# Performance work log

Measured on AMD Instinct MI355X. Metric: run time of the kernel, lower is better.

Reference implementation:

```python
import jax, jax.numpy as jnp
import numpy as np

IN_FEATURES = 8192
OUT_FEATURES = 8192
POOL_K = 16
SCALE = 2.0


def setup_inputs() -> dict:
    key = jax.random.key(0)
    k1, k2, k3 = jax.random.split(key, 3)
    B = 4096
    x = jax.random.normal(k1, (B, IN_FEATURES), dtype=jnp.float32)
    # nn.Linear default init: U(-1/sqrt(fan_in), 1/sqrt(fan_in))
    bound = 1.0 / np.sqrt(IN_FEATURES)
    W = jax.random.uniform(k2, (OUT_FEATURES, IN_FEATURES), dtype=jnp.float32, minval=-bound, maxval=bound)
    b = jax.random.uniform(k3, (OUT_FEATURES,), dtype=jnp.float32, minval=-bound, maxval=bound)
    return {"x": x, "W": W, "b": b}


def reference(x, W, b):
    # GEMM: [B, C_out]
    y = jnp.dot(x, W.T) + b
    B, C = y.shape
    # AvgPool1d over feature dim, kernel=stride=POOL_K -> [B, C/POOL_K]
    pooled = y.reshape(B, C // POOL_K, POOL_K).mean(axis=-1)
    # GELU (tanh approximation) + scale, then row-wise max -> [B]
    v = jax.nn.gelu(pooled, approximate=True) * SCALE
    return jnp.max(v, axis=-1)
```

## Files before the change

### kernel.cpp

```cpp
#include <hip/hip_runtime.h>
#include <hip/hip_bf16.h>
#include <cmath>

#define M_DIM 4096
#define N_POOL 512
#define K_DIM 8192
#define KSPLIT 4
#define K_PER (K_DIM / KSPLIT)

typedef __bf16 bf16x8 __attribute__((ext_vector_type(8)));
typedef float floatx4 __attribute__((ext_vector_type(4)));
typedef unsigned short ushort8v __attribute__((ext_vector_type(8)));

__device__ __forceinline__ unsigned short f2bf(float f) {
  unsigned int u = __float_as_uint(f);
  return (unsigned short)((u + 0x7fffu + ((u >> 16) & 1u)) >> 16);
}

__global__ void convert_f32_bf16(const float4* __restrict__ src,
                                 ushort8v* __restrict__ dst, int n8,
                                 const float* __restrict__ b,
                                 float* __restrict__ bpool) {
  if (blockIdx.x == gridDim.x - 1) {
    for (int g = threadIdx.x; g < N_POOL; g += blockDim.x) {
      float s = 0.f;
#pragma unroll
      for (int i = 0; i < 16; ++i) s += b[g * 16 + i];
      bpool[g] = s;
    }
    return;
  }
  int i = blockIdx.x * blockDim.x + threadIdx.x;
  int stride = (gridDim.x - 1) * blockDim.x;
  for (; i < n8; i += stride) {
    float4 a = src[2 * i], c = src[2 * i + 1];
    ushort8v o;
    o[0] = f2bf(a.x); o[1] = f2bf(a.y); o[2] = f2bf(a.z); o[3] = f2bf(a.w);
    o[4] = f2bf(c.x); o[5] = f2bf(c.y); o[6] = f2bf(c.z); o[7] = f2bf(c.w);
    dst[i] = o;
  }
}

__global__ void wpool_kernel(const float* __restrict__ W,
                             unsigned short* __restrict__ Wp) {
  int g = blockIdx.x;
  const float* base = W + (size_t)g * 16 * K_DIM;
  ushort4* out = (ushort4*)(Wp + (size_t)g * K_DIM);
  for (int c4 = threadIdx.x; c4 < K_DIM / 4; c4 += blockDim.x) {
    float4 s = {0.f, 0.f, 0.f, 0.f};
#pragma unroll
    for (int j = 0; j < 16; ++j) {
      float4 v = ((const float4*)(base + (size_t)j * K_DIM))[c4];
      s.x += v.x; s.y += v.y; s.z += v.z; s.w += v.w;
    }
    ushort4 o;
    o.x = f2bf(s.x); o.y = f2bf(s.y); o.z = f2bf(s.z); o.w = f2bf(s.w);
    out[c4] = o;
  }
}

__global__ __launch_bounds__(256) void gemm_splitk(
    const unsigned short* __restrict__ xb,
    const unsigned short* __restrict__ wp,
    float* __restrict__ part)
{
  __shared__ __align__(16) unsigned short As[128 * 64];
  __shared__ __align__(16) unsigned short Bs[128 * 64];

  const int tid = threadIdx.x;
  const int L = tid & 63;
  const int w = tid >> 6;
  const int wm = w & 1, wn = w >> 1;
  const int lane15 = L & 15, quad = L >> 4;

  const int id = blockIdx.x;
  const int xcd = id & 7;
  const int c = id >> 3;
  const int kz = xcd >> 1;
  const int j = (c << 1) | (xcd & 1);
  const int bn = j & 3, bm = j >> 2;

  const int srow = w * 32 + (L >> 3);
  const int schunk = ((L & 7) ^ ((L >> 3) & 7)) * 8;
  const unsigned short* ga = xb + (size_t)(bm * 128 + srow) * K_DIM + kz * K_PER + schunk;
  const unsigned short* gb = wp + (size_t)(bn * 128 + srow) * K_DIM + kz * K_PER + schunk;
  unsigned short* lA = As + (w * 32) * 64;
  unsigned short* lB = Bs + (w * 32) * 64;

  floatx4 acc[4][4];
#pragma unroll
  for (int t = 0; t < 4; ++t)
#pragma unroll
    for (int u = 0; u < 4; ++u) acc[t][u] = (floatx4)0.f;

  const bf16x8* Av = (const bf16x8*)As;
  const bf16x8* Bv = (const bf16x8*)Bs;

  for (int kk = 0; kk < K_PER / 64; ++kk) {
#pragma unroll
    for (int i = 0; i < 4; ++i) {
      __builtin_amdgcn_global_load_lds(
          (const __attribute__((address_space(1))) void*)(ga + (size_t)(i * 8) * K_DIM),
          (__attribute__((address_space(3))) void*)(lA + i * 8 * 64), 16, 0, 0);
    }
#pragma unroll
    for (int i = 0; i < 4; ++i) {
      __builtin_amdgcn_global_load_lds(
          (const __attribute__((address_space(1))) void*)(gb + (size_t)(i * 8) * K_DIM),
          (__attribute__((address_space(3))) void*)(lB + i * 8 * 64), 16, 0, 0);
    }
    ga += 64; gb += 64;
    __syncthreads();

#pragma unroll
    for (int ks = 0; ks < 2; ++ks) {
      bf16x8 af[4], bfr[4];
#pragma unroll
      for (int t = 0; t < 4; ++t) {
        int r = wm * 64 + t * 16 + lane15;
        af[t] = Av[r * 8 + ((ks * 4 + quad) ^ (lane15 & 7))];
      }
#pragma unroll
      for (int u = 0; u < 4; ++u) {
        int r = wn * 64 + u * 16 + lane15;
        bfr[u] = Bv[r * 8 + ((ks * 4 + quad) ^ (lane15 & 7))];
      }
#pragma unroll
      for (int t = 0; t < 4; ++t)
#pragma unroll
        for (int u = 0; u < 4; ++u)
          acc[t][u] = __builtin_amdgcn_mfma_f32_16x16x32_bf16(af[t], bfr[u],
                                                              acc[t][u], 0, 0, 0);
    }
    __syncthreads();
  }

  float* cp = part + (size_t)kz * M_DIM * N_POOL;
  const int row_base = bm * 128 + wm * 64;
  const int col_base = bn * 128 + wn * 64;
#pragma unroll
  for (int t = 0; t < 4; ++t)
#pragma unroll
    for (int u = 0; u < 4; ++u) {
      int col = col_base + u * 16 + lane15;
#pragma unroll
      for (int r = 0; r < 4; ++r) {
        int row = row_base + t * 16 + quad * 4 + r;
        cp[(size_t)row * N_POOL + col] = acc[t][u][r];
      }
    }
}

__device__ __forceinline__ float gelu2(float s) {
  float p = s * 0.0625f;
  float t = tanhf(0.7978845608028654f * (p + 0.044715f * p * p * p));
  return p * (1.0f + t);
}

__global__ void finalize(const float* __restrict__ part,
                         const float* __restrict__ bpool,
                         float* __restrict__ out) {
  const int w = threadIdx.x >> 6, lane = threadIdx.x & 63;
  const int row = blockIdx.x * 4 + w;
  const float4* bp4 = (const float4*)bpool;
  float mx = -INFINITY;
#pragma unroll
  for (int j = 0; j < 2; ++j) {
    int g4 = lane + j * 64;
    float4 s = bp4[g4];
#pragma unroll
    for (int kz = 0; kz < KSPLIT; ++kz) {
      float4 v = ((const float4*)(part + (size_t)kz * M_DIM * N_POOL +
                                  (size_t)row * N_POOL))[g4];
      s.x += v.x; s.y += v.y; s.z += v.z; s.w += v.w;
    }
    mx = fmaxf(mx, fmaxf(fmaxf(gelu2(s.x), gelu2(s.y)),
                         fmaxf(gelu2(s.z), gelu2(s.w))));
  }
#pragma unroll
  for (int sh = 32; sh >= 1; sh >>= 1) mx = fmaxf(mx, __shfl_xor(mx, sh));
  if (lane == 0) out[row] = mx;
}

extern "C" void kernel_launch(void* const* d_in, const int* in_sizes, int n_in,
                              void* d_out, int out_size, void* d_ws, size_t ws_size,
                              hipStream_t stream) {
  const float* x = (const float*)d_in[0];
  const float* W = (const float*)d_in[1];
  const float* b = (const float*)d_in[2];
  float* out = (float*)d_out;

  char* ws = (char*)d_ws;
  unsigned short* xb = (unsigned short*)ws;
  unsigned short* Wp = (unsigned short*)(ws + (size_t)67108864);
  float* part = (float*)(ws + (size_t)75497472);
  float* bpool = (float*)(ws + (size_t)109051904);

  wpool_kernel<<<N_POOL, 256, 0, stream>>>(W, Wp);
  convert_f32_bf16<<<2049, 256, 0, stream>>>((const float4*)x, (ushort8v*)xb,
                                             (M_DIM * K_DIM) / 8, b, bpool);

  gemm_splitk<<<512, 256, 0, stream>>>(xb, Wp, part);

  finalize<<<M_DIM / 4, 256, 0, stream>>>(part, bpool, out);
}
```

Measured before the change: 496.6 us.

## Fuse prep kernels into one launch and raise split-K to eight

Merges the weight-pooling, input bf16 conversion and bias pooling into a single prep kernel so there is one launch instead of two and the phases can overlap. Split-K goes from 4 to 8, which doubles the GEMM grid to 1024 blocks to fill more CUs, and the block-to-XCD mapping now puts each K slice on its own XCD. The cost is a larger fp32 partial buffer that finalize must read and sum, and bpool is moved to a later workspace offset to make room for it.

```diff
diff --git a/kernel.cpp b/kernel.cpp
--- a/kernel.cpp
+++ b/kernel.cpp
@@ -5,7 +5,7 @@
 #define M_DIM 4096
 #define N_POOL 512
 #define K_DIM 8192
-#define KSPLIT 4
+#define KSPLIT 8
 #define K_PER (K_DIM / KSPLIT)
 
 typedef __bf16 bf16x8 __attribute__((ext_vector_type(8)));
@@ -17,45 +17,46 @@
   return (unsigned short)((u + 0x7fffu + ((u >> 16) & 1u)) >> 16);
 }
 
-__global__ void convert_f32_bf16(const float4* __restrict__ src,
-                                 ushort8v* __restrict__ dst, int n8,
-                                 const float* __restrict__ b,
-                                 float* __restrict__ bpool) {
-  if (blockIdx.x == gridDim.x - 1) {
+#define WPOOL_BLOCKS 512
+#define CONV_BLOCKS 2048
+
+__global__ __launch_bounds__(256) void prep_kernel(
+    const float* __restrict__ W, unsigned short* __restrict__ Wp,
+    const float4* __restrict__ src, ushort8v* __restrict__ dst, int n8,
+    const float* __restrict__ b, float* __restrict__ bpool) {
+  int bid = blockIdx.x;
+  if (bid < WPOOL_BLOCKS) {
+    int g = bid;
+    const float* base = W + (size_t)g * 16 * K_DIM;
+    ushort4* out = (ushort4*)(Wp + (size_t)g * K_DIM);
+    for (int c4 = threadIdx.x; c4 < K_DIM / 4; c4 += blockDim.x) {
+      float4 s = {0.f, 0.f, 0.f, 0.f};
+#pragma unroll
+      for (int j = 0; j < 16; ++j) {
+        float4 v = ((const float4*)(base + (size_t)j * K_DIM))[c4];
+        s.x += v.x; s.y += v.y; s.z += v.z; s.w += v.w;
+      }
+      ushort4 o;
+      o.x = f2bf(s.x); o.y = f2bf(s.y); o.z = f2bf(s.z); o.w = f2bf(s.w);
+      out[c4] = o;
+    }
+  } else if (bid < WPOOL_BLOCKS + CONV_BLOCKS) {
+    int i = (bid - WPOOL_BLOCKS) * blockDim.x + threadIdx.x;
+    int stride = CONV_BLOCKS * blockDim.x;
+    for (; i < n8; i += stride) {
+      float4 a = src[2 * i], c = src[2 * i + 1];
+      ushort8v o;
+      o[0] = f2bf(a.x); o[1] = f2bf(a.y); o[2] = f2bf(a.z); o[3] = f2bf(a.w);
+      o[4] = f2bf(c.x); o[5] = f2bf(c.y); o[6] = f2bf(c.z); o[7] = f2bf(c.w);
+      dst[i] = o;
+    }
+  } else {
     for (int g = threadIdx.x; g < N_POOL; g += blockDim.x) {
       float s = 0.f;
 #pragma unroll
       for (int i = 0; i < 16; ++i) s += b[g * 16 + i];
       bpool[g] = s;
     }
-    return;
-  }
-  int i = blockIdx.x * blockDim.x + threadIdx.x;
-  int stride = (gridDim.x - 1) * blockDim.x;
-  for (; i < n8; i += stride) {
-    float4 a = src[2 * i], c = src[2 * i + 1];
-    ushort8v o;
-    o[0] = f2bf(a.x); o[1] = f2bf(a.y); o[2] = f2bf(a.z); o[3] = f2bf(a.w);
-    o[4] = f2bf(c.x); o[5] = f2bf(c.y); o[6] = f2bf(c.z); o[7] = f2bf(c.w);
-    dst[i] = o;
-  }
-}
-
-__global__ void wpool_kernel(const float* __restrict__ W,
-                             unsigned short* __restrict__ Wp) {
-  int g = blockIdx.x;
-  const float* base = W + (size_t)g * 16 * K_DIM;
-  ushort4* out = (ushort4*)(Wp + (size_t)g * K_DIM);
-  for (int c4 = threadIdx.x; c4 < K_DIM / 4; c4 += blockDim.x) {
-    float4 s = {0.f, 0.f, 0.f, 0.f};
-#pragma unroll
-    for (int j = 0; j < 16; ++j) {
-      float4 v = ((const float4*)(base + (size_t)j * K_DIM))[c4];
-      s.x += v.x; s.y += v.y; s.z += v.z; s.w += v.w;
-    }
-    ushort4 o;
-    o.x = f2bf(s.x); o.y = f2bf(s.y); o.z = f2bf(s.z); o.w = f2bf(s.w);
-    out[c4] = o;
   }
 }
 
@@ -74,11 +75,9 @@
   const int lane15 = L & 15, quad = L >> 4;
 
   const int id = blockIdx.x;
-  const int xcd = id & 7;
+  const int kz = id & 7;
   const int c = id >> 3;
-  const int kz = xcd >> 1;
-  const int j = (c << 1) | (xcd & 1);
-  const int bn = j & 3, bm = j >> 2;
+  const int bn = c & 3, bm = c >> 2;
 
   const int srow = w * 32 + (L >> 3);
   const int schunk = ((L & 7) ^ ((L >> 3) & 7)) * 8;
@@ -194,13 +193,12 @@
   unsigned short* xb = (unsigned short*)ws;
   unsigned short* Wp = (unsigned short*)(ws + (size_t)67108864);
   float* part = (float*)(ws + (size_t)75497472);
-  float* bpool = (float*)(ws + (size_t)109051904);
-
-  wpool_kernel<<<N_POOL, 256, 0, stream>>>(W, Wp);
-  convert_f32_bf16<<<2049, 256, 0, stream>>>((const float4*)x, (ushort8v*)xb,
-                                             (M_DIM * K_DIM) / 8, b, bpool);
-
-  gemm_splitk<<<512, 256, 0, stream>>>(xb, Wp, part);
+  float* bpool = (float*)(ws + (size_t)142606336);
+
+  prep_kernel<<<WPOOL_BLOCKS + CONV_BLOCKS + 1, 256, 0, stream>>>(
+      W, Wp, (const float4*)x, (ushort8v*)xb, (M_DIM * K_DIM) / 8, b, bpool);
+
+  gemm_splitk<<<1024, 256, 0, stream>>>(xb, Wp, part);
 
   finalize<<<M_DIM / 4, 256, 0, stream>>>(part, bpool, out);
 }
```

Result: no change. 502.6 us (+1.2%).
